# Performance work log

Measured on AMD Instinct MI355X. Metric: run time of the kernel, lower is better.

## Reference

```python
import jax, jax.numpy as jnp
import numpy as np

B, C, T, V = 8, 64, 16, 207
H, WSZ = 8, 4
EPS = 1e-5


def setup_inputs() -> dict:
    key = jax.random.key(0)
    ks = jax.random.split(key, 16)
    def w(k, shape):
        return jax.random.normal(k, shape, jnp.float32) * 0.02
    inp = {"x": jax.random.normal(ks[0], (B, C, T, V), jnp.float32)}
    for i, s in enumerate("ab"):
        o = 1 + i * 4
        inp[f"qkv_w_{s}"] = w(ks[o], (C, 3 * C))
        inp[f"qkv_b_{s}"] = jnp.zeros((3 * C,), jnp.float32)
        inp[f"proj_w_{s}"] = w(ks[o + 1], (C, C))
        inp[f"proj_b_{s}"] = jnp.zeros((C,), jnp.float32)
        inp[f"ffn_w1_{s}"] = w(ks[o + 2], (C, 4 * C))
        inp[f"ffn_b1_{s}"] = jnp.zeros((4 * C,), jnp.float32)
        inp[f"ffn_w2_{s}"] = w(ks[o + 3], (4 * C, C))
        inp[f"ffn_b2_{s}"] = jnp.zeros((C,), jnp.float32)
        inp[f"ln_{s}1_g"] = jnp.ones((C, T, V), jnp.float32)
        inp[f"ln_{s}1_b"] = jnp.zeros((C, T, V), jnp.float32)
        inp[f"ln_{s}2_g"] = jnp.ones((C, T, V), jnp.float32)
        inp[f"ln_{s}2_b"] = jnp.zeros((C, T, V), jnp.float32)
    inp["n_head"] = H
    inp["window_size"] = WSZ
    return inp


def _layer_norm(x, g, b):
    # LayerNorm over (C, T, V) dims of [B, C, T, V]
    mu = jnp.mean(x, axis=(1, 2, 3), keepdims=True)
    var = jnp.var(x, axis=(1, 2, 3), keepdims=True)
    return (x - mu) / jnp.sqrt(var + EPS) * g + b


def _window_att(x, wqkv, bqkv, wo, bo, n_head, wsz):
    # Joint spatio-temporal attention within windows of `wsz` timesteps.
    b_, c_, t_, v_ = x.shape
    nw = t_ // wsz
    dh = c_ // n_head
    # [B,C,T,V] -> [B,T,V,C] -> [B,nW, wsz*V, C]
    xt = jnp.transpose(x, (0, 2, 3, 1)).reshape(b_, nw, wsz * v_, c_)
    qkv = xt @ wqkv + bqkv  # [B,nW,N,3C]
    q, k, v = jnp.split(qkv, 3, axis=-1)
    def heads(t):
        return t.reshape(b_, nw, -1, n_head, dh).transpose(0, 1, 3, 2, 4)  # [B,nW,H,N,dh]
    q, k, v = heads(q), heads(k), heads(v)
    scale = 1.0 / jnp.sqrt(jnp.asarray(dh, jnp.float32))
    att = jax.nn.softmax(jnp.einsum('bwhnd,bwhmd->bwhnm', q, k) * scale, axis=-1)
    out = jnp.einsum('bwhnm,bwhmd->bwhnd', att, v)
    out = out.transpose(0, 1, 3, 2, 4).reshape(b_, nw, wsz * v_, c_) @ wo + bo
    return out.reshape(b_, t_, v_, c_).transpose(0, 3, 1, 2)


def _ffn(x, w1, b1, w2, b2):
    h = jax.nn.relu(jnp.einsum('bctv,cd->bdtv', x, w1) + b1[None, :, None, None])
    return jnp.einsum('bdtv,dc->bctv', h, w2) + b2[None, :, None, None]


def _block(x, wqkv, bqkv, wo, bo, w1, b1, w2, b2, g1, be1, g2, be2, n_head, wsz):
    x = _window_att(x, wqkv, bqkv, wo, bo, n_head, wsz) + x
    x = _layer_norm(x, g1, be1)
    x = _ffn(x, w1, b1, w2, b2) + x
    x = _layer_norm(x, g2, be2)
    # cyclic shift along time by shift_pixel = wsz // 2
    return jnp.roll(x, -(wsz // 2), axis=2)


def reference(x, qkv_w_a, qkv_b_a, proj_w_a, proj_b_a, ffn_w1_a, ffn_b1_a, ffn_w2_a, ffn_b2_a,
              ln_a1_g, ln_a1_b, ln_a2_g, ln_a2_b,
              qkv_w_b, qkv_b_b, proj_w_b, proj_b_b, ffn_w1_b, ffn_b1_b, ffn_w2_b, ffn_b2_b,
              ln_b1_g, ln_b1_b, ln_b2_g, ln_b2_b, n_head, window_size):
    x = _block(x, qkv_w_a, qkv_b_a, proj_w_a, proj_b_a, ffn_w1_a, ffn_b1_a, ffn_w2_a, ffn_b2_a,
               ln_a1_g, ln_a1_b, ln_a2_g, ln_a2_b, n_head, window_size)
    x = _block(x, qkv_w_b, qkv_b_b, proj_w_b, proj_b_b, ffn_w1_b, ffn_b1_b, ffn_w2_b, ffn_b2_b,
               ln_b1_g, ln_b1_b, ln_b2_g, ln_b2_b, n_head, window_size)
    return x
```

## Files before the change

### kernel.cpp

```cpp
#include <hip/hip_runtime.h>
#include <hip/hip_bf16.h>

#define Bb  8
#define Cc  64
#define Tt  16
#define Vv  207
#define Hh  8
#define DH  8
#define NW  4
#define WSZ 4
#define Nn  (WSZ*Vv)
#define NP  832
#define TV  (Tt*Vv)
#define CTV (Cc*Tt*Vv)
#define S   (Bb*CTV)
#define NBWH (Bb*NW*Hh)
#define EPSF 1e-5f
#define QSCALE 0.51006971401146f
#define FRAG_BWH (52*64*4)
#define LAYER_WSZ 49152

typedef __attribute__((ext_vector_type(4))) short bf16x4;
typedef __attribute__((ext_vector_type(4))) float f32x4;
typedef __attribute__((ext_vector_type(2))) unsigned int u32x2;
typedef __attribute__((ext_vector_type(4))) unsigned int u32x4;

static __device__ __forceinline__ short f2bf(float f) {
    union { float f; unsigned u; } v; v.f = f;
    unsigned r = (v.u + 0x7FFFu + ((v.u >> 16) & 1u)) >> 16;
    return (short)r;
}

static __device__ __forceinline__ bf16x4 pack4(float a, float b, float c, float d) {
    unsigned ua = __builtin_bit_cast(unsigned, a) + 0x8000u;
    unsigned ub = __builtin_bit_cast(unsigned, b) + 0x8000u;
    unsigned uc = __builtin_bit_cast(unsigned, c) + 0x8000u;
    unsigned ud = __builtin_bit_cast(unsigned, d) + 0x8000u;
    u32x2 t;
    t[0] = (ua >> 16) | (ub & 0xFFFF0000u);
    t[1] = (uc >> 16) | (ud & 0xFFFF0000u);
    return __builtin_bit_cast(bf16x4, t);
}

__global__ void prep_kernel(const float* __restrict__ qa, const float* __restrict__ pa,
                            const float* __restrict__ w1a, const float* __restrict__ w2a,
                            const float* __restrict__ qbw, const float* __restrict__ pbw,
                            const float* __restrict__ w1b, const float* __restrict__ w2b,
                            short* __restrict__ wf, float* __restrict__ stats,
                            short* __restrict__ qf, short* __restrict__ kf,
                            short* __restrict__ vf) {
    int i0 = blockIdx.x*256 + threadIdx.x;
    if (i0 < 64) stats[i0] = 0.f;
    for (int i = i0; i < 24576; i += 416*256) {
        int l = i / 12288; int f = i % 12288;
        const float* qw = l ? qbw : qa;
        const float* pw = l ? pbw : pa;
        const float* w1 = l ? w1b : w1a;
        const float* w2 = l ? w2b : w2a;
        short* dst = wf + l*LAYER_WSZ;
        bf16x4 out;
        if (f < 3072) {
            int s = f; int nt = s>>8; int kc = (s>>6)&3; int ln = s&63;
            int li = ln&15; int q = ln>>4;
            #pragma unroll
            for (int j = 0; j < 4; ++j) out[j] = f2bf(qw[(kc*16+q*4+j)*192 + nt*16+li]);
            *((bf16x4*)&dst[s*4]) = out;
        } else if (f < 4096) {
            int s = f-3072; int nt = s>>8; int kc = (s>>6)&3; int ln = s&63;
            int li = ln&15; int q = ln>>4;
            #pragma unroll
            for (int j = 0; j < 4; ++j) out[j] = f2bf(pw[(kc*16+q*4+j)*64 + nt*16+li]);
            *((bf16x4*)&dst[12288 + s*4]) = out;
        } else if (f < 8192) {
            int s = f-4096; int nt = s>>8; int kc = (s>>6)&3; int ln = s&63;
            int li = ln&15; int q = ln>>4;
            #pragma unroll
            for (int j = 0; j < 4; ++j) out[j] = f2bf(w1[(kc*16+q*4+j)*256 + nt*16+li]);
            *((bf16x4*)&dst[16384 + s*4]) = out;
        } else {
            int s = f-8192; int nt = s>>8; int ct = (s>>6)&3; int ln = s&63;
            int li = ln&15; int q = ln>>4;
            #pragma unroll
            for (int j = 0; j < 4; ++j) out[j] = f2bf(w2[(nt*16+q*4+j)*64 + ct*16+li]);
            *((bf16x4*)&dst[32768 + s*4]) = out;
        }
    }
    for (int i = i0; i < NBWH*1664; i += 416*256) {
        int bwh = i / 1664; int rest = i % 1664;
        int nt = rest >> 5; int u = rest & 31;
        size_t base = (size_t)bwh*FRAG_BWH + nt*256;
        *((u32x2*)&qf[base + (32+u)*4]) = (u32x2){0u,0u};
        *((u32x2*)&kf[base + (32+u)*4]) = (u32x2){0u,0u};
        int vlane = (u>>3)*16 + 8 + (u&7);
        short v = ((u&7) == 0) ? (short)0x3F80 : (short)0;
        bf16x4 vv4 = {v,v,v,v};
        *((bf16x4*)&vf[base + vlane*4]) = vv4;
    }
}

__global__ __launch_bounds__(512) void qkv_kernel(const float* __restrict__ src,
        const float* __restrict__ st, const float* __restrict__ g, const float* __restrict__ be,
        const short* __restrict__ wfq, const float* __restrict__ bias,
        short* __restrict__ qf, short* __restrict__ kf, short* __restrict__ vf) {
    __shared__ short wqs[12288];
    __shared__ float bqs[192];
    __shared__ short os[64*196];
    int tid = threadIdx.x;
    int b = blockIdx.x / 52;
    int r0 = (blockIdx.x % 52) * 64;
    const float* xb = src + (size_t)b*CTV;
    {
        const u32x2* wsrc = (const u32x2*)wfq;
        u32x2* wdst = (u32x2*)wqs;
        for (int s = tid; s < 3072; s += 512) wdst[s] = wsrc[s];
    }
    if (tid < 192) bqs[tid] = bias[tid];
    __syncthreads();

    int lane = tid & 63; int wv = tid >> 6;
    int rs = wv & 3; int gsel = wv >> 2;
    int l15 = lane & 15; int quad = lane >> 4;
    int r = r0 + rs*16 + l15;
    int rc = (r < TV) ? r : TV-1;
    int t = rc / Vv; int vv = rc - t*Vv;
    float mean = 0.f, rstd = 0.f; int off;
    if (st) {
        mean = st[b*2] * (1.0f/CTV);
        float var = st[b*2+1] * (1.0f/CTV) - mean*mean;
        rstd = rsqrtf(var + EPSF);
        off = ((t+2)&15)*Vv + vv;
    } else off = rc;

    bf16x4 xf[4];
    #pragma unroll
    for (int kc = 0; kc < 4; ++kc) {
        #pragma unroll
        for (int j = 0; j < 4; ++j) {
            int idx = (kc*16 + quad*4 + j)*TV + off;
            float xv = xb[idx];
            if (st) xv = (xv - mean)*rstd*g[idx] + be[idx];
            xf[kc][j] = f2bf(xv);
        }
    }

    f32x4 accv[6];
    #pragma unroll
    for (int ntl = 0; ntl < 6; ++ntl) {
        int nt = gsel*6 + ntl;
        float4 bb = *((const float4*)&bqs[nt*16 + quad*4]);
        f32x4 acc = {bb.x, bb.y, bb.z, bb.w};
        #pragma unroll
        for (int kc = 0; kc < 4; ++kc) {
            bf16x4 wf2 = *((const bf16x4*)&wqs[((nt*4 + kc)*64 + lane)*4]);
            acc = __builtin_amdgcn_mfma_f32_16x16x16bf16_1k(wf2, xf[kc], acc, 0, 0, 0);
        }
        accv[ntl] = acc;
    }

    int pos = rs*16 + l15;
    #pragma unroll
    for (int ntl = 0; ntl < 6; ++ntl) {
        int nt = gsel*6 + ntl;
        f32x4 a = accv[ntl];
        bf16x4 pk = (nt < 4) ? pack4(a[0]*QSCALE, a[1]*QSCALE, a[2]*QSCALE, a[3]*QSCALE)
                             : pack4(a[0], a[1], a[2], a[3]);
        *((bf16x4*)&os[pos*196 + nt*16 + quad*4]) = pk;
    }
    __syncthreads();

    int pp = tid & 63;
    int rr = r0 + pp;
    bool pv = rr < TV;
    int rrc = pv ? rr : TV-1;
    int t4 = rrc / Vv; int vv4 = rrc - t4*Vv;
    int n2 = (t4 & 3)*Vv + vv4;
    int nt2 = n2 >> 4; int l15n = n2 & 15;
    int quadn = (n2 & 15) >> 2; int jn = n2 & 3;
    int wbase = (b*NW + (t4 >> 2))*Hh;
    if (pv) {
        {
            int h = wv;
            size_t fb = ((size_t)(wbase+h)*52 + nt2)*256;
            bf16x4 q0 = *((const bf16x4*)&os[pp*196 + h*8]);
            bf16x4 q1 = *((const bf16x4*)&os[pp*196 + h*8 + 4]);
            *((bf16x4*)&qf[fb + l15n*4])        = q0;
            *((bf16x4*)&qf[fb + (16 + l15n)*4]) = q1;
            bf16x4 k0 = *((const bf16x4*)&os[pp*196 + 64 + h*8]);
            bf16x4 k1 = *((const bf16x4*)&os[pp*196 + 64 + h*8 + 4]);
            *((bf16x4*)&kf[fb + l15n*4])        = k0;
            *((bf16x4*)&kf[fb + (16 + l15n)*4]) = k1;
        }
        #pragma unroll
        for (int i = 0; i < 8; ++i) {
            int hd = i*8 + wv;
            int h = hd >> 3; int d = hd & 7;
            vf[(((size_t)(wbase+h)*52 + nt2)*64 + quadn*16 + d)*4 + jn]
                = os[pp*196 + 128 + hd];
        }
    }
}

__global__ __launch_bounds__(1024) void attn_kernel(const short* __restrict__ qf,
        const short* __restrict__ kf, const short* __restrict__ vf,
        short* __restrict__ att) {
    __shared__ short ks2[FRAG_BWH];
    __shared__ short vs2[FRAG_BWH];
    int bwh = blockIdx.x;
    int tid = threadIdx.x;
    int lane = tid & 63;
    int wv = tid >> 6;
    int quad = lane >> 4;
    int l15 = lane & 15;

    {
        const u32x4* kg = (const u32x4*)(kf + (size_t)bwh*FRAG_BWH);
        const u32x4* vg = (const u32x4*)(vf + (size_t)bwh*FRAG_BWH);
        u32x4* kd = (u32x4*)ks2; u32x4* vd = (u32x4*)vs2;
        for (int idx = tid; idx < 1664; idx += 1024) { kd[idx] = kg[idx]; vd[idx] = vg[idx]; }
    }
    __syncthreads();

    int nm = (wv < 4) ? 4 : 3;
    const short* qbase = qf + (size_t)bwh*FRAG_BWH;
    bf16x4 aq[4];
    f32x4 oacc[4];
    #pragma unroll
    for (int i = 0; i < 4; ++i) {
        aq[i] = (bf16x4){0,0,0,0};
        oacc[i] = (f32x4){0.f,0.f,0.f,0.f};
        if (i < nm)
            aq[i] = *(const bf16x4*)(qbase + ((wv + 16*i)*256 + lane*4));
    }

    for (int nt = 0; nt < 52; ++nt) {
        bf16x4 ak = *(const bf16x4*)&ks2[nt*256 + lane*4];
        bf16x4 av = *(const bf16x4*)&vs2[nt*256 + lane*4];
        bool mask = (nt == 51) && (quad == 3);
        #pragma unroll
        for (int i = 0; i < 4; ++i) {
            if (i < nm) {
                f32x4 s = __builtin_amdgcn_mfma_f32_16x16x16bf16_1k(
                              ak, aq[i], (f32x4){0.f,0.f,0.f,0.f}, 0, 0, 0);
                bf16x4 pb = pack4(__builtin_amdgcn_exp2f(s[0]), __builtin_amdgcn_exp2f(s[1]),
                                  __builtin_amdgcn_exp2f(s[2]), __builtin_amdgcn_exp2f(s[3]));
                if (mask) pb = (bf16x4){0,0,0,0};
                oacc[i] = __builtin_amdgcn_mfma_f32_16x16x16bf16_1k(av, pb, oacc[i], 0, 0, 0);
            }
        }
    }
    int h = bwh & 7; int bw = bwh >> 3;
    #pragma unroll
    for (int i = 0; i < 4; ++i) {
        if (i < nm) {
            float ls = __shfl(oacc[i][0], 32 + l15, 64);
            float inv = 1.f / ls;
            int m = (wv + 16*i)*16 + l15;
            if (quad < 2 && m < Nn) {
                bf16x4 ov = pack4(oacc[i][0]*inv, oacc[i][1]*inv,
                                  oacc[i][2]*inv, oacc[i][3]*inv);
                *((bf16x4*)&att[((size_t)bw*Nn + m)*Cc + h*DH + quad*4]) = ov;
            }
        }
    }
}

__global__ __launch_bounds__(512) void proj_kernel(const short* __restrict__ att,
        const short* __restrict__ wfp, const float* __restrict__ bo,
        const float* __restrict__ resid,
        const float* __restrict__ st, const float* __restrict__ g, const float* __restrict__ be,
        float* __restrict__ out, float* __restrict__ stats) {
    __shared__ short wos[4096];
    __shared__ float bos[64];
    __shared__ float r1[512], r2[512];
    int tid = threadIdx.x;
    int b = blockIdx.x / 52;
    int r0 = (blockIdx.x % 52) * 64;
    const float* xb = resid + (size_t)b*CTV;
    {
        const u32x2* wsrc = (const u32x2*)wfp;
        u32x2* wdst = (u32x2*)wos;
        for (int s = tid; s < 1024; s += 512) wdst[s] = wsrc[s];
    }
    if (tid < 64) bos[tid] = bo[tid];
    __syncthreads();

    int lane = tid & 63; int wv = tid >> 6;
    int rs = wv & 3; int gsel = wv >> 2;
    int l15 = lane & 15; int quad = lane >> 4;
    int r = r0 + rs*16 + l15;
    bool valid = r < TV;
    int rc = valid ? r : TV-1;
    int t = rc / Vv; int vv = rc - t*Vv;
    int n = (t & 3)*Vv + vv;
    int bw = b*NW + (t >> 2);
    const short* arow = att + ((size_t)bw*Nn + n)*Cc;
    bf16x4 af[4];
    #pragma unroll
    for (int kc = 0; kc < 4; ++kc)
        af[kc] = *((const bf16x4*)&arow[kc*16 + quad*4]);

    f32x4 acc[2];
    #pragma unroll
    for (int ntl = 0; ntl < 2; ++ntl) {
        int nt = gsel*2 + ntl;
        float4 bb = *((const float4*)&bos[nt*16 + quad*4]);
        acc[ntl] = (f32x4){bb.x, bb.y, bb.z, bb.w};
        #pragma unroll
        for (int kc = 0; kc < 4; ++kc) {
            bf16x4 wf2 = *((const bf16x4*)&wos[((nt*4 + kc)*64 + lane)*4]);
            acc[ntl] = __builtin_amdgcn_mfma_f32_16x16x16bf16_1k(wf2, af[kc], acc[ntl], 0, 0, 0);
        }
    }
    float mean = 0.f, rstd = 0.f; int off;
    if (st) {
        mean = st[b*2] * (1.0f/CTV);
        float var = st[b*2+1] * (1.0f/CTV) - mean*mean;
        rstd = rsqrtf(var + EPSF);
        off = ((t+2)&15)*Vv + vv;
    } else off = rc;
    float s1 = 0.f, s2 = 0.f;
    if (valid) {
        #pragma unroll
        for (int ntl = 0; ntl < 2; ++ntl) {
            int nt = gsel*2 + ntl;
            #pragma unroll
            for (int j = 0; j < 4; ++j) {
                int c_out = nt*16 + quad*4 + j;
                int ridx = c_out*TV + off;
                float xv = xb[ridx];
                if (st) xv = (xv - mean)*rstd*g[ridx] + be[ridx];
                float val = acc[ntl][j] + xv;
                out[(size_t)b*CTV + (size_t)c_out*TV + r] = val;
                s1 += val; s2 += val*val;
            }
        }
    }
    r1[tid] = s1; r2[tid] = s2;
    __syncthreads();
    for (int o = 256; o > 0; o >>= 1) {
        if (tid < o) { r1[tid] += r1[tid+o]; r2[tid] += r2[tid+o]; }
        __syncthreads();
    }
    if (tid == 0) { atomicAdd(&stats[b*2], r1[0]); atomicAdd(&stats[b*2+1], r2[0]); }
}

__global__ void ln_apply_kernel(const float* __restrict__ x,
                                const float* __restrict__ g,
                                const float* __restrict__ be,
                                const float* __restrict__ stats,
                                float* __restrict__ out,
                                int shift) {
    int idx = blockIdx.x*256 + threadIdx.x;
    if (idx >= S) return;
    int b = idx / CTV; int r = idx % CTV;
    int c = r / TV; int q2 = r % TV; int t = q2 / Vv; int vv = q2 % Vv;
    float mean = stats[b*2] * (1.0f/CTV);
    float var  = stats[b*2+1] * (1.0f/CTV) - mean*mean;
    float rstd = rsqrtf(var + EPSF);
    float val = (x[idx]-mean)*rstd*g[r] + be[r];
    int tout = (t - shift + Tt) % Tt;
    size_t oidx = ((size_t)(b*Cc + c)*Tt + tout)*Vv + vv;
    out[oidx] = val;
}

__global__ __launch_bounds__(512) void ffn_kernel(const float* __restrict__ xin,
        const float* __restrict__ st, const float* __restrict__ g, const float* __restrict__ be,
        const short* __restrict__ wf1, const float* __restrict__ b1,
        const short* __restrict__ wf2g, const float* __restrict__ b2,
        float* __restrict__ out, float* __restrict__ stats) {
    __shared__ short w1s[16384];
    __shared__ short w2s[16384];
    __shared__ short xsf[4096];
    __shared__ float b1s[256];
    __shared__ float b2s[64];
    __shared__ float r1s[512], r2s[512];
    int tid = threadIdx.x;
    int b = blockIdx.x / 52;
    int r0 = (blockIdx.x % 52) * 64;
    const float* xb = xin + (size_t)b*CTV;
    float mean = st[b*2] * (1.0f/CTV);
    float var  = st[b*2+1] * (1.0f/CTV) - mean*mean;
    float rstd = rsqrtf(var + EPSF);

    {
        const u32x2* s1p = (const u32x2*)wf1;
        const u32x2* s2p = (const u32x2*)wf2g;
        u32x2* d1 = (u32x2*)w1s; u32x2* d2 = (u32x2*)w2s;
        for (int s = tid; s < 4096; s += 512) { d1[s] = s1p[s]; d2[s] = s2p[s]; }
    }
    for (int s2 = tid; s2 < 1024; s2 += 512) {
        int wv2 = s2 >> 8; int kc = (s2 >> 6) & 3; int ln = s2 & 63;
        int l15 = ln & 15; int quad = ln >> 4;
        int r = r0 + wv2*16 + l15; if (r >= TV) r = TV-1;
        bf16x4 f;
        #pragma unroll
        for (int j = 0; j < 4; ++j) {
            int idx = (kc*16 + quad*4 + j)*TV + r;
            f[j] = f2bf((xb[idx] - mean)*rstd*g[idx] + be[idx]);
        }
        *((bf16x4*)&xsf[s2*4]) = f;
    }
    if (tid < 256) b1s[tid] = b1[tid];
    if (tid < 64) b2s[tid] = b2[tid];
    __syncthreads();

    int lane = tid & 63; int wv = tid >> 6;
    int rs = wv & 3; int gsel = wv >> 2;
    int l15 = lane & 15; int quad = lane >> 4;
    bf16x4 xf[4];
    #pragma unroll
    for (int kc = 0; kc < 4; ++kc)
        xf[kc] = *((const bf16x4*)&xsf[((rs*4 + kc)*64 + lane)*4]);

    f32x4 oacc[2];
    #pragma unroll
    for (int ctl = 0; ctl < 2; ++ctl) oacc[ctl] = (f32x4){0.f,0.f,0.f,0.f};

    for (int nt = 0; nt < 16; ++nt) {
        float4 bb = *((const float4*)&b1s[nt*16 + quad*4]);
        f32x4 acc = {bb.x, bb.y, bb.z, bb.w};
        #pragma unroll
        for (int kc = 0; kc < 4; ++kc) {
            bf16x4 wfv = *((const bf16x4*)&w1s[((nt*4 + kc)*64 + lane)*4]);
            acc = __builtin_amdgcn_mfma_f32_16x16x16bf16_1k(wfv, xf[kc], acc, 0, 0, 0);
        }
        bf16x4 pf = pack4(fmaxf(acc[0], 0.f), fmaxf(acc[1], 0.f),
                          fmaxf(acc[2], 0.f), fmaxf(acc[3], 0.f));
        #pragma unroll
        for (int ctl = 0; ctl < 2; ++ctl) {
            int ct = gsel*2 + ctl;
            bf16x4 wfv2 = *((const bf16x4*)&w2s[((nt*4 + ct)*64 + lane)*4]);
            oacc[ctl] = __builtin_amdgcn_mfma_f32_16x16x16bf16_1k(wfv2, pf, oacc[ctl], 0, 0, 0);
        }
    }
    int r = r0 + rs*16 + l15;
    float s1 = 0.f, s2v = 0.f;
    if (r < TV) {
        #pragma unroll
        for (int ctl = 0; ctl < 2; ++ctl) {
            int ct = gsel*2 + ctl;
            #pragma unroll
            for (int j = 0; j < 4; ++j) {
                int c_out = ct*16 + quad*4 + j;
                int idx = c_out*TV + r;
                float xv = (xb[idx] - mean)*rstd*g[idx] + be[idx];
                float val = oacc[ctl][j] + b2s[c_out] + xv;
                out[(size_t)b*CTV + idx] = val;
                s1 += val; s2v += val*val;
            }
        }
    }
    r1s[tid] = s1; r2s[tid] = s2v;
    __syncthreads();
    for (int o = 256; o > 0; o >>= 1) {
        if (tid < o) { r1s[tid] += r1s[tid+o]; r2s[tid] += r2s[tid+o]; }
        __syncthreads();
    }
    if (tid == 0) { atomicAdd(&stats[b*2], r1s[0]); atomicAdd(&stats[b*2+1], r2s[0]); }
}

extern "C" void kernel_launch(void* const* d_in, const int* in_sizes, int n_in,
                              void* d_out, int out_size, void* d_ws, size_t ws_size,
                              hipStream_t stream) {
    const float* xin = (const float*)d_in[0];

    float* bufA  = (float*)d_ws;
    float* bufB  = bufA + S;
    float* stats = bufB + S;
    short* qf    = (short*)(stats + 64);
    short* kf    = qf + (size_t)NBWH*FRAG_BWH;
    short* vf    = kf + (size_t)NBWH*FRAG_BWH;
    short* att   = vf + (size_t)NBWH*FRAG_BWH;
    short* wf    = att + (size_t)32*Nn*64;

    const float* A0  = (const float*)d_in[1];
    const float* A1  = (const float*)d_in[2];
    const float* A2  = (const float*)d_in[3];
    const float* A3  = (const float*)d_in[4];
    const float* A4  = (const float*)d_in[5];
    const float* A5  = (const float*)d_in[6];
    const float* A6  = (const float*)d_in[7];
    const float* A7  = (const float*)d_in[8];
    const float* A8  = (const float*)d_in[9];
    const float* A9  = (const float*)d_in[10];
    const float* A10 = (const float*)d_in[11];
    const float* A11 = (const float*)d_in[12];
    const float* B0  = (const float*)d_in[13];
    const float* B1  = (const float*)d_in[14];
    const float* B2  = (const float*)d_in[15];
    const float* B3  = (const float*)d_in[16];
    const float* B4  = (const float*)d_in[17];
    const float* B5  = (const float*)d_in[18];
    const float* B6  = (const float*)d_in[19];
    const float* B7  = (const float*)d_in[20];
    const float* B8  = (const float*)d_in[21];
    const float* B9  = (const float*)d_in[22];
    const float* B10 = (const float*)d_in[23];
    const float* B11 = (const float*)d_in[24];

    float* st1a = stats + 0;
    float* st2a = stats + 16;
    float* st1b = stats + 32;
    float* st2b = stats + 48;

    short* wfA = wf;
    short* wfB = wf + LAYER_WSZ;

    prep_kernel<<<416, 256, 0, stream>>>(A0, A2, A4, A6, B0, B2, B4, B6,
                                         wf, stats, qf, kf, vf);

    qkv_kernel<<<Bb*52, 512, 0, stream>>>(xin, nullptr, nullptr, nullptr,
                                          wfA, A1, qf, kf, vf);
    attn_kernel<<<NBWH, 1024, 0, stream>>>(qf, kf, vf, att);
    proj_kernel<<<Bb*52, 512, 0, stream>>>(att, wfA + 12288, A3, xin,
                                           nullptr, nullptr, nullptr, bufB, st1a);
    ffn_kernel<<<Bb*52, 512, 0, stream>>>(bufB, st1a, A8, A9,
                                          wfA + 16384, A5, wfA + 32768, A7, bufB, st2a);
    qkv_kernel<<<Bb*52, 512, 0, stream>>>(bufB, st2a, A10, A11,
                                          wfB, B1, qf, kf, vf);
    attn_kernel<<<NBWH, 1024, 0, stream>>>(qf, kf, vf, att);
    proj_kernel<<<Bb*52, 512, 0, stream>>>(att, wfB + 12288, B3, bufB,
                                           st2a, A10, A11, bufA, st1b);
    ffn_kernel<<<Bb*52, 512, 0, stream>>>(bufA, st1b, B8, B9,
                                          wfB + 16384, B5, wfB + 32768, B7, bufA, st2b);
    ln_apply_kernel<<<(S+255)/256, 256, 0, stream>>>(bufA, B10, B11, st2b, (float*)d_out, WSZ/2);
}
```

Measured before the change: 280.3 us.

## Fuse weight prep into consumer kernels and vectorize final LayerNorm apply

Removes the separate prep kernel: each qkv/proj/ffn block now converts its fp32 weights to bf16 MFMA fragment layout directly into shared memory, and the first qkv launch also does the stats and padding initialization, including extra zeroing of tail-tile fragments. The point is to drop one kernel launch and the round trip of pre-converted weights through global memory. In exchange, every block redoes the strided fp32 gather and conversion of the weights. The final ln_apply kernel now handles four elements per thread with a float4 load and a hardcoded shift. The attention loop is also marked unroll 1.

```diff
diff --git a/kernel.cpp b/kernel.cpp
--- a/kernel.cpp
+++ b/kernel.cpp
@@ -10,7 +10,6 @@
 #define NW  4
 #define WSZ 4
 #define Nn  (WSZ*Vv)
-#define NP  832
 #define TV  (Tt*Vv)
 #define CTV (Cc*Tt*Vv)
 #define S   (Bb*CTV)
@@ -18,7 +17,6 @@
 #define EPSF 1e-5f
 #define QSCALE 0.51006971401146f
 #define FRAG_BWH (52*64*4)
-#define LAYER_WSZ 49152
 
 typedef __attribute__((ext_vector_type(4))) short bf16x4;
 typedef __attribute__((ext_vector_type(4))) float f32x4;
@@ -42,66 +40,11 @@
     return __builtin_bit_cast(bf16x4, t);
 }
 
-__global__ void prep_kernel(const float* __restrict__ qa, const float* __restrict__ pa,
-                            const float* __restrict__ w1a, const float* __restrict__ w2a,
-                            const float* __restrict__ qbw, const float* __restrict__ pbw,
-                            const float* __restrict__ w1b, const float* __restrict__ w2b,
-                            short* __restrict__ wf, float* __restrict__ stats,
-                            short* __restrict__ qf, short* __restrict__ kf,
-                            short* __restrict__ vf) {
-    int i0 = blockIdx.x*256 + threadIdx.x;
-    if (i0 < 64) stats[i0] = 0.f;
-    for (int i = i0; i < 24576; i += 416*256) {
-        int l = i / 12288; int f = i % 12288;
-        const float* qw = l ? qbw : qa;
-        const float* pw = l ? pbw : pa;
-        const float* w1 = l ? w1b : w1a;
-        const float* w2 = l ? w2b : w2a;
-        short* dst = wf + l*LAYER_WSZ;
-        bf16x4 out;
-        if (f < 3072) {
-            int s = f; int nt = s>>8; int kc = (s>>6)&3; int ln = s&63;
-            int li = ln&15; int q = ln>>4;
-            #pragma unroll
-            for (int j = 0; j < 4; ++j) out[j] = f2bf(qw[(kc*16+q*4+j)*192 + nt*16+li]);
-            *((bf16x4*)&dst[s*4]) = out;
-        } else if (f < 4096) {
-            int s = f-3072; int nt = s>>8; int kc = (s>>6)&3; int ln = s&63;
-            int li = ln&15; int q = ln>>4;
-            #pragma unroll
-            for (int j = 0; j < 4; ++j) out[j] = f2bf(pw[(kc*16+q*4+j)*64 + nt*16+li]);
-            *((bf16x4*)&dst[12288 + s*4]) = out;
-        } else if (f < 8192) {
-            int s = f-4096; int nt = s>>8; int kc = (s>>6)&3; int ln = s&63;
-            int li = ln&15; int q = ln>>4;
-            #pragma unroll
-            for (int j = 0; j < 4; ++j) out[j] = f2bf(w1[(kc*16+q*4+j)*256 + nt*16+li]);
-            *((bf16x4*)&dst[16384 + s*4]) = out;
-        } else {
-            int s = f-8192; int nt = s>>8; int ct = (s>>6)&3; int ln = s&63;
-            int li = ln&15; int q = ln>>4;
-            #pragma unroll
-            for (int j = 0; j < 4; ++j) out[j] = f2bf(w2[(nt*16+q*4+j)*64 + ct*16+li]);
-            *((bf16x4*)&dst[32768 + s*4]) = out;
-        }
-    }
-    for (int i = i0; i < NBWH*1664; i += 416*256) {
-        int bwh = i / 1664; int rest = i % 1664;
-        int nt = rest >> 5; int u = rest & 31;
-        size_t base = (size_t)bwh*FRAG_BWH + nt*256;
-        *((u32x2*)&qf[base + (32+u)*4]) = (u32x2){0u,0u};
-        *((u32x2*)&kf[base + (32+u)*4]) = (u32x2){0u,0u};
-        int vlane = (u>>3)*16 + 8 + (u&7);
-        short v = ((u&7) == 0) ? (short)0x3F80 : (short)0;
-        bf16x4 vv4 = {v,v,v,v};
-        *((bf16x4*)&vf[base + vlane*4]) = vv4;
-    }
-}
-
 __global__ __launch_bounds__(512) void qkv_kernel(const float* __restrict__ src,
         const float* __restrict__ st, const float* __restrict__ g, const float* __restrict__ be,
-        const short* __restrict__ wfq, const float* __restrict__ bias,
-        short* __restrict__ qf, short* __restrict__ kf, short* __restrict__ vf) {
+        const float* __restrict__ qw, const float* __restrict__ bias,
+        short* __restrict__ qf, short* __restrict__ kf, short* __restrict__ vf,
+        float* __restrict__ stats, int doInit) {
     __shared__ short wqs[12288];
     __shared__ float bqs[192];
     __shared__ short os[64*196];
@@ -109,13 +52,6 @@
     int b = blockIdx.x / 52;
     int r0 = (blockIdx.x % 52) * 64;
     const float* xb = src + (size_t)b*CTV;
-    {
-        const u32x2* wsrc = (const u32x2*)wfq;
-        u32x2* wdst = (u32x2*)wqs;
-        for (int s = tid; s < 3072; s += 512) wdst[s] = wsrc[s];
-    }
-    if (tid < 192) bqs[tid] = bias[tid];
-    __syncthreads();
 
     int lane = tid & 63; int wv = tid >> 6;
     int rs = wv & 3; int gsel = wv >> 2;
@@ -137,11 +73,49 @@
         #pragma unroll
         for (int j = 0; j < 4; ++j) {
             int idx = (kc*16 + quad*4 + j)*TV + off;
-            float xv = xb[idx];
-            if (st) xv = (xv - mean)*rstd*g[idx] + be[idx];
-            xf[kc][j] = f2bf(xv);
-        }
-    }
+            float x0 = xb[idx];
+            if (st) x0 = (x0 - mean)*rstd*g[idx] + be[idx];
+            xf[kc][j] = f2bf(x0);
+        }
+    }
+
+    for (int fs = tid; fs < 3072; fs += 512) {
+        int nt = fs >> 8; int kc = (fs >> 6) & 3; int ln = fs & 63;
+        int li = ln & 15; int q = ln >> 4;
+        bf16x4 o;
+        #pragma unroll
+        for (int j = 0; j < 4; ++j) o[j] = f2bf(qw[(kc*16 + q*4 + j)*192 + nt*16 + li]);
+        *((bf16x4*)&wqs[fs*4]) = o;
+    }
+    if (tid < 192) bqs[tid] = bias[tid];
+
+    if (doInit) {
+        if (blockIdx.x == 0 && tid < 64) stats[tid] = 0.f;
+        for (int i = blockIdx.x*512 + tid; i < NBWH*1664; i += 416*512) {
+            int bwh = i / 1664; int rest = i % 1664;
+            int nt = rest >> 5; int u = rest & 31;
+            size_t base = (size_t)bwh*FRAG_BWH + nt*256;
+            *((u32x2*)&qf[base + (32+u)*4]) = (u32x2){0u, 0u};
+            *((u32x2*)&kf[base + (32+u)*4]) = (u32x2){0u, 0u};
+            int vlane = (u>>3)*16 + 8 + (u&7);
+            short v = ((u&7) == 0) ? (short)0x3F80 : (short)0;
+            bf16x4 vv4 = {v,v,v,v};
+            *((bf16x4*)&vf[base + vlane*4]) = vv4;
+            if (nt == 51) {
+                bf16x4 z4 = {0,0,0,0};
+                if (u < 4) {
+                    *((bf16x4*)&kf[base + (12+u)*4]) = z4;
+                    *((bf16x4*)&qf[base + (12+u)*4]) = z4;
+                } else if (u < 8) {
+                    *((bf16x4*)&kf[base + (24+u)*4]) = z4;
+                    *((bf16x4*)&qf[base + (24+u)*4]) = z4;
+                } else if (u < 16) {
+                    *((bf16x4*)&vf[base + (40+u)*4]) = z4;
+                }
+            }
+        }
+    }
+    __syncthreads();
 
     f32x4 accv[6];
     #pragma unroll
@@ -232,6 +206,7 @@
             aq[i] = *(const bf16x4*)(qbase + ((wv + 16*i)*256 + lane*4));
     }
 
+    #pragma unroll 1
     for (int nt = 0; nt < 52; ++nt) {
         bf16x4 ak = *(const bf16x4*)&ks2[nt*256 + lane*4];
         bf16x4 av = *(const bf16x4*)&vs2[nt*256 + lane*4];
@@ -265,7 +240,7 @@
 }
 
 __global__ __launch_bounds__(512) void proj_kernel(const short* __restrict__ att,
-        const short* __restrict__ wfp, const float* __restrict__ bo,
+        const float* __restrict__ pw, const float* __restrict__ bo,
         const float* __restrict__ resid,
         const float* __restrict__ st, const float* __restrict__ g, const float* __restrict__ be,
         float* __restrict__ out, float* __restrict__ stats) {
@@ -276,13 +251,6 @@
     int b = blockIdx.x / 52;
     int r0 = (blockIdx.x % 52) * 64;
     const float* xb = resid + (size_t)b*CTV;
-    {
-        const u32x2* wsrc = (const u32x2*)wfp;
-        u32x2* wdst = (u32x2*)wos;
-        for (int s = tid; s < 1024; s += 512) wdst[s] = wsrc[s];
-    }
-    if (tid < 64) bos[tid] = bo[tid];
-    __syncthreads();
 
     int lane = tid & 63; int wv = tid >> 6;
     int rs = wv & 3; int gsel = wv >> 2;
@@ -298,6 +266,17 @@
     #pragma unroll
     for (int kc = 0; kc < 4; ++kc)
         af[kc] = *((const bf16x4*)&arow[kc*16 + quad*4]);
+
+    for (int fs = tid; fs < 1024; fs += 512) {
+        int nt = fs >> 8; int kc = (fs >> 6) & 3; int ln = fs & 63;
+        int li = ln & 15; int q = ln >> 4;
+        bf16x4 o;
+        #pragma unroll
+        for (int j = 0; j < 4; ++j) o[j] = f2bf(pw[(kc*16 + q*4 + j)*64 + nt*16 + li]);
+        *((bf16x4*)&wos[fs*4]) = o;
+    }
+    if (tid < 64) bos[tid] = bo[tid];
+    __syncthreads();
 
     f32x4 acc[2];
     #pragma unroll
@@ -348,25 +327,30 @@
                                 const float* __restrict__ g,
                                 const float* __restrict__ be,
                                 const float* __restrict__ stats,
-                                float* __restrict__ out,
-                                int shift) {
-    int idx = blockIdx.x*256 + threadIdx.x;
-    if (idx >= S) return;
-    int b = idx / CTV; int r = idx % CTV;
-    int c = r / TV; int q2 = r % TV; int t = q2 / Vv; int vv = q2 % Vv;
+                                float* __restrict__ out) {
+    int i4 = (blockIdx.x*256 + threadIdx.x) * 4;
+    if (i4 >= S) return;
+    int b = i4 / CTV; int r = i4 % CTV;
+    int c = r / TV; int q2 = r % TV; int t = q2 / Vv; int vv = q2 - t*Vv;
     float mean = stats[b*2] * (1.0f/CTV);
     float var  = stats[b*2+1] * (1.0f/CTV) - mean*mean;
     float rstd = rsqrtf(var + EPSF);
-    float val = (x[idx]-mean)*rstd*g[r] + be[r];
-    int tout = (t - shift + Tt) % Tt;
-    size_t oidx = ((size_t)(b*Cc + c)*Tt + tout)*Vv + vv;
-    out[oidx] = val;
+    float4 xv = *((const float4*)&x[i4]);
+    float vals[4] = {xv.x, xv.y, xv.z, xv.w};
+    size_t obase = (size_t)(b*Cc + c)*Tt;
+    #pragma unroll
+    for (int j = 0; j < 4; ++j) {
+        float val = (vals[j]-mean)*rstd*g[r+j] + be[r+j];
+        int tout = (t - 2 + Tt) & 15;
+        out[(obase + tout)*Vv + vv] = val;
+        if (++vv == Vv) { vv = 0; ++t; }
+    }
 }
 
 __global__ __launch_bounds__(512) void ffn_kernel(const float* __restrict__ xin,
         const float* __restrict__ st, const float* __restrict__ g, const float* __restrict__ be,
-        const short* __restrict__ wf1, const float* __restrict__ b1,
-        const short* __restrict__ wf2g, const float* __restrict__ b2,
+        const float* __restrict__ w1r, const float* __restrict__ b1,
+        const float* __restrict__ w2r, const float* __restrict__ b2,
         float* __restrict__ out, float* __restrict__ stats) {
     __shared__ short w1s[16384];
     __shared__ short w2s[16384];
@@ -382,12 +366,6 @@
     float var  = st[b*2+1] * (1.0f/CTV) - mean*mean;
     float rstd = rsqrtf(var + EPSF);
 
-    {
-        const u32x2* s1p = (const u32x2*)wf1;
-        const u32x2* s2p = (const u32x2*)wf2g;
-        u32x2* d1 = (u32x2*)w1s; u32x2* d2 = (u32x2*)w2s;
-        for (int s = tid; s < 4096; s += 512) { d1[s] = s1p[s]; d2[s] = s2p[s]; }
-    }
     for (int s2 = tid; s2 < 1024; s2 += 512) {
         int wv2 = s2 >> 8; int kc = (s2 >> 6) & 3; int ln = s2 & 63;
         int l15 = ln & 15; int quad = ln >> 4;
@@ -399,6 +377,18 @@
             f[j] = f2bf((xb[idx] - mean)*rstd*g[idx] + be[idx]);
         }
         *((bf16x4*)&xsf[s2*4]) = f;
+    }
+    for (int fs = tid; fs < 4096; fs += 512) {
+        int nt = fs >> 8; int kc = (fs >> 6) & 3; int ln = fs & 63;
+        int li = ln & 15; int q = ln >> 4;
+        bf16x4 o1;
+        #pragma unroll
+        for (int j = 0; j < 4; ++j) o1[j] = f2bf(w1r[(kc*16 + q*4 + j)*256 + nt*16 + li]);
+        *((bf16x4*)&w1s[fs*4]) = o1;
+        bf16x4 o2;
+        #pragma unroll
+        for (int j = 0; j < 4; ++j) o2[j] = f2bf(w2r[(nt*16 + q*4 + j)*64 + kc*16 + li]);
+        *((bf16x4*)&w2s[fs*4]) = o2;
     }
     if (tid < 256) b1s[tid] = b1[tid];
     if (tid < 64) b2s[tid] = b2[tid];
@@ -471,7 +461,6 @@
     short* kf    = qf + (size_t)NBWH*FRAG_BWH;
     short* vf    = kf + (size_t)NBWH*FRAG_BWH;
     short* att   = vf + (size_t)NBWH*FRAG_BWH;
-    short* wf    = att + (size_t)32*Nn*64;
 
     const float* A0  = (const float*)d_in[1];
     const float* A1  = (const float*)d_in[2];
@@ -503,25 +492,19 @@
     float* st1b = stats + 32;
     float* st2b = stats + 48;
 
-    short* wfA = wf;
-    short* wfB = wf + LAYER_WSZ;
-
-    prep_kernel<<<416, 256, 0, stream>>>(A0, A2, A4, A6, B0, B2, B4, B6,
-                                         wf, stats, qf, kf, vf);
-
     qkv_kernel<<<Bb*52, 512, 0, stream>>>(xin, nullptr, nullptr, nullptr,
-                                          wfA, A1, qf, kf, vf);
+                                          A0, A1, qf, kf, vf, stats, 1);
     attn_kernel<<<NBWH, 1024, 0, stream>>>(qf, kf, vf, att);
-    proj_kernel<<<Bb*52, 512, 0, stream>>>(att, wfA + 12288, A3, xin,
+    proj_kernel<<<Bb*52, 512, 0, stream>>>(att, A2, A3, xin,
                                            nullptr, nullptr, nullptr, bufB, st1a);
     ffn_kernel<<<Bb*52, 512, 0, stream>>>(bufB, st1a, A8, A9,
-                                          wfA + 16384, A5, wfA + 32768, A7, bufB, st2a);
+                                          A4, A5, A6, A7, bufB, st2a);
     qkv_kernel<<<Bb*52, 512, 0, stream>>>(bufB, st2a, A10, A11,
-                                          wfB, B1, qf, kf, vf);
+                                          B0, B1, qf, kf, vf, stats, 0);
     attn_kernel<<<NBWH, 1024, 0, stream>>>(qf, kf, vf, att);
-    proj_kernel<<<Bb*52, 512, 0, stream>>>(att, wfB + 12288, B3, bufB,
+    proj_kernel<<<Bb*52, 512, 0, stream>>>(att, B2, B3, bufB,
                                            st2a, A10, A11, bufA, st1b);
     ffn_kernel<<<Bb*52, 512, 0, stream>>>(bufA, st1b, B8, B9,
-                                          wfB + 16384, B5, wfB + 32768, B7, bufA, st2b);
-    ln_apply_kernel<<<(S+255)/256, 256, 0, stream>>>(bufA, B10, B11, st2b, (float*)d_out, WSZ/2);
-}
+                                          B4, B5, B6, B7, bufA, st2b);
+    ln_apply_kernel<<<(S/4+255)/256, 256, 0, stream>>>(bufA, B10, B11, st2b, (float*)d_out);
+}
```

After: 285.5 us. Within noise of the previous version (+1.8%).
